# Kernel optimization log

Hardware: AMD Instinct MI355X
Metric: run time of the kernel (lower is better)

## Reference

```python
import jax, jax.numpy as jnp
import numpy as np

B, V, SX, SY, TIN = 4, 3, 256, 256, 10
WIDTH, M1, M2, STEP, VOUT, NL = 32, 16, 16, 10, 3, 6


def setup_inputs() -> dict:
    key = jax.random.key(0)
    ks = jax.random.split(key, 20)
    n = lambda k, s, sc=1.0: sc * jax.random.normal(k, s, dtype=jnp.float32)
    u = lambda k, s: jax.random.uniform(k, s, dtype=jnp.float32)
    sc = 1.0 / WIDTH
    cshape = (NL, WIDTH, WIDTH, V, M1, M2)
    return {
        'x': n(ks[0], (B, V, SX, SY, TIN)),
        'fc0_w': n(ks[1], (TIN + 2, WIDTH), 0.1), 'fc0_b': jnp.zeros((WIDTH,), jnp.float32),
        'w1r': sc * u(ks[2], cshape), 'w1i': sc * u(ks[3], cshape),
        'w2r': sc * u(ks[4], cshape), 'w2i': sc * u(ks[5], cshape),
        'm1w': n(ks[6], (NL, WIDTH, WIDTH), 0.05), 'm1b': jnp.zeros((NL, WIDTH), jnp.float32),
        'm2w': n(ks[7], (NL, WIDTH, WIDTH), 0.05), 'm2b': jnp.zeros((NL, WIDTH), jnp.float32),
        'ww': n(ks[8], (NL, WIDTH, WIDTH), 0.05), 'wb': jnp.zeros((NL, WIDTH), jnp.float32),
        'bw': n(ks[9], (NL, WIDTH, 2), 0.1), 'bb': jnp.zeros((NL, WIDTH), jnp.float32),
        'fc1v_w': n(ks[10], (V, VOUT), 0.3), 'fc1v_b': jnp.zeros((VOUT,), jnp.float32),
        'fc1t_w': n(ks[11], (WIDTH, 256), 0.05), 'fc1t_b': jnp.zeros((256,), jnp.float32),
        'fc2t_w': n(ks[12], (256, STEP), 0.05), 'fc2t_b': jnp.zeros((STEP,), jnp.float32),
    }


def _gelu(t):
    return jax.nn.gelu(t, approximate=False)  # torch F.gelu default = exact erf


def _conv1x1(x, w, b):
    # 1x1x1 Conv3d: channel mix only. x: (b,c,v,x,y), w: (out,in)
    return jnp.einsum('bcvxy,oc->bovxy', x, w) + b[None, :, None, None, None]


def _spectral(x, w1, w2):
    # x: (b,c,v,X,Y); rfft2 over (X,Y); mode-truncated complex mix, zero-pad, irfft2
    sx, sy = x.shape[-2], x.shape[-1]
    xf = jnp.fft.rfft2(x)  # (b,c,v,X,Y//2+1) complex64
    o1 = jnp.einsum('bivxy,iovxy->bovxy', xf[..., :M1, :M2], w1)
    o2 = jnp.einsum('bivxy,iovxy->bovxy', xf[..., -M1:, :M2], w2)
    out = jnp.zeros((x.shape[0], w1.shape[1]) + xf.shape[2:], jnp.complex64)
    out = out.at[..., :M1, :M2].set(o1).at[..., -M1:, :M2].set(o2)
    return jnp.fft.irfft2(out, s=(sx, sy))


def reference(x, fc0_w, fc0_b, w1r, w1i, w2r, w2i, m1w, m1b, m2w, m2b, ww, wb, bw, bb,
              fc1v_w, fc1v_b, fc1t_w, fc1t_b, fc2t_w, fc2t_b):
    b, v, sx, sy, _ = x.shape
    gx = jnp.broadcast_to(jnp.linspace(0.0, 1.0, sx, dtype=jnp.float32)[:, None], (sx, sy))
    gy = jnp.broadcast_to(jnp.linspace(0.0, 1.0, sy, dtype=jnp.float32)[None, :], (sx, sy))
    grid = jnp.broadcast_to(jnp.stack([gx, gy], -1)[None, None], (b, v, sx, sy, 2))
    h = jnp.concatenate([x, grid], -1) @ fc0_w + fc0_b  # (b,v,X,Y,C)
    h = h.transpose(0, 4, 1, 2, 3)  # (b,C,v,X,Y)
    g = grid.transpose(0, 4, 1, 2, 3)  # (b,2,v,X,Y)

    def layer(i, t):
        x1 = _spectral(t, w1r[i] + 1j * w1i[i], w2r[i] + 1j * w2i[i])
        x1 = _conv1x1(_gelu(_conv1x1(x1, m1w[i], m1b[i])), m2w[i], m2b[i])
        x2 = _conv1x1(t, ww[i], wb[i])
        x3 = _conv1x1(g, bw[i], bb[i])
        return _gelu(x1 + x2 + x3)

    h0 = layer(0, h)
    h = layer(1, h0)
    h = layer(2, h) + h0
    h1 = layer(3, h)
    h = layer(4, h1)
    h = layer(5, h) + h1

    h = h.transpose(0, 1, 3, 4, 2)  # (b,C,X,Y,v)
    h = _gelu(h @ fc1v_w + fc1v_b)
    h = h.transpose(0, 4, 2, 3, 1)  # (b,vout,X,Y,C)
    h = _gelu(h @ fc1t_w + fc1t_b)
    return h @ fc2t_w + fc2t_b  # (b,vout,X,Y,step)
```

## Files before the change

### kernel.cpp

```cpp
#include <hip/hip_runtime.h>
#include <math.h>


#define OFF_A   0
#define OFF_B   25165824
#define OFF_T   50331648
#define OFF_XF  53477376
#define OFF_T1  54263808
#define OFF_T2T 54272000
#define OFF_TCS 54288384
#define OFF_TB  54304768
#define OFF_WT  54312960
#define OFF_FW  54321152
#define FWSZ    4718592
#define WS_NEED_WT   ((size_t)OFF_FW * 4)
#define WS_NEED_FOLD ((size_t)(OFF_FW + 4*FWSZ) * 4)

__device__ __forceinline__ float geluf(float x) {
    float a = fabsf(x) * 0.70710678118654752f;
    float t = __builtin_amdgcn_rcpf(fmaf(0.3275911f, a, 1.0f));
    float p = t * fmaf(t, fmaf(t, fmaf(t, fmaf(t, 1.061405429f, -1.453152027f),
                                       1.421413741f), -0.284496736f), 0.254829592f);
    float e = __expf(-a * a);
    float erfa = fmaf(-p, e, 1.0f);
    float er = copysignf(erfa, x);
    return 0.5f * x * (1.0f + er);
}

__global__ void k_init_tables(float* __restrict__ ws, const float* __restrict__ w1t, int do_wt) {
    const float W0 = 6.2831853071795864769f / 256.0f;
    int stride = gridDim.x * blockDim.x;
    int tid = blockIdx.x * blockDim.x + threadIdx.x;
    for (int i = tid; i < 4096; i += stride) {
        int m = i >> 5, q = i & 31, g = q >> 2, j = q & 3;
        int k0 = 4 * (g & 3) + (g >> 2);
        int k = k0 + 2 * (j >> 1);
        float th = W0 * (float)((k * m) & 255);
        ws[OFF_T1 + i] = (j & 1) ? -sinf(th) : cosf(th);
    }
    for (int idx = tid; idx < 8192; idx += stride) {
        int n = idx >> 5, kx = idx & 31;
        int KX = (kx < 16) ? kx : (kx + 224);
        float th = W0 * (float)((KX * n) & 255);
        ws[OFF_T2T + 2*idx]     = cosf(th);
        ws[OFF_T2T + 2*idx + 1] = sinf(th);
    }
    for (int idx = tid; idx < 8192; idx += stride) {
        int kx = idx >> 8, n = idx & 255;
        int KX = (kx < 16) ? kx : (kx + 224);
        float th = W0 * (float)((KX * n) & 255);
        ws[OFF_TCS + 2*idx]     = cosf(th);
        ws[OFF_TCS + 2*idx + 1] = sinf(th);
    }
    for (int idx = tid; idx < 8192; idx += stride) {
        int j = idx >> 8, m = idx & 255, k = j >> 1;
        float th = W0 * (float)((k * m) & 255);
        float beta = (k == 0) ? (1.0f/65536.0f) : (2.0f/65536.0f);
        float val;
        if (j & 1) val = (k == 0) ? 0.0f : -beta * sinf(th);
        else       val = beta * cosf(th);
        ws[OFF_TB + idx] = val;
    }
    if (do_wt) {
        for (int idx = tid; idx < 8192; idx += stride)
            ws[OFF_WT + idx] = w1t[(idx & 31) * 256 + (idx >> 5)];
    }
}

__global__ __launch_bounds__(256) void k_foldw(const float* __restrict__ w1r,
                                               const float* __restrict__ w1i,
                                               const float* __restrict__ w2r,
                                               const float* __restrict__ w2i,
                                               const float* __restrict__ m1w,
                                               float2* __restrict__ fp1,
                                               float2* __restrict__ fp2) {
    int blk = blockIdx.x;
    int p = threadIdx.x;
    int op = blk & 31; int li = blk >> 5;
    int l = li >> 5;
    const float* mrow = m1w + l*1024 + op*32;
#pragma unroll
    for (int v = 0; v < 3; ++v) {
        float a1r = 0.f, a1i = 0.f, a2r = 0.f, a2i = 0.f;
#pragma unroll 4
        for (int o = 0; o < 32; ++o) {
            float mw = mrow[o];
            size_t idx = ((size_t)(li*32 + o)*3 + v)*256 + p;
            a1r = fmaf(mw, w1r[idx], a1r); a1i = fmaf(mw, w1i[idx], a1i);
            a2r = fmaf(mw, w2r[idx], a2r); a2i = fmaf(mw, w2i[idx], a2i);
        }
        size_t oidx = ((size_t)(li*32 + op)*3 + v)*256 + p;
        float2 u1; u1.x = a1r; u1.y = a1i;
        float2 u2; u2.x = a2r; u2.y = a2i;
        fp1[oidx] = u1; fp2[oidx] = u2;
    }
}

__device__ __forceinline__ void fold_lds(float* lds, int tid) {
#pragma unroll
    for (int it = 0; it < 16; ++it) {
        int pi = it * 256 + tid;
        int r = pi >> 7, mm = pi & 127;
        float* row = lds + r * 257;
        float a = row[mm], c = row[mm + 128];
        row[mm] = a + c; row[mm + 128] = a - c;
    }
}

__device__ __forceinline__ void dft_row_phase(const float* lds, const float* __restrict__ tabF,
                                              float* __restrict__ T, int b, int v, int n, int tid) {
    int r = tid >> 3, g = tid & 7;
    int p = g >> 2, idx = g & 3;
    const float* dp = lds + r * 257 + p * 128;
    const float* tp = tabF + g * 4;
    float a0 = 0.f, a1 = 0.f, a2 = 0.f, a3 = 0.f;
#pragma unroll 4
    for (int m = 0; m < 128; ++m) {
        float d = dp[m];
        float4 t = *(const float4*)(tp + m * 32);
        a0 += d * t.x; a1 += d * t.y; a2 += d * t.z; a3 += d * t.w;
    }
    size_t trow = ((size_t)((b * 32 + r) * 3 + v) * 256 + n) * 32;
    float2 w0; w0.x = a0; w0.y = a1;
    float2 w1; w1.x = a2; w1.y = a3;
    *(float2*)(T + trow + 8 * idx + 2 * p) = w0;
    *(float2*)(T + trow + 8 * idx + 2 * p + 4) = w1;
}

__global__ __launch_bounds__(256) void k_fc0(const float* __restrict__ x,
                                             const float* __restrict__ w,
                                             const float* __restrict__ bias,
                                             float* __restrict__ outA,
                                             float* __restrict__ T,
                                             const float* __restrict__ tabF) {
    __shared__ float lds[32 * 257];
    int blk = blockIdx.x;
    int m = threadIdx.x;
    int n = blk & 255;
    int bv = blk >> 8;
    int v = bv % 3, b = bv / 3;
    const float* xp = x + ((size_t)blk * 256 + m) * 10;
    float xin[10];
#pragma unroll
    for (int t = 0; t < 10; t++) xin[t] = xp[t];
    float gx = (float)n * (1.0f/255.0f), gy = (float)m * (1.0f/255.0f);
    float* op = outA + ((size_t)(b*96) + v) * 65536 + n * 256 + m;
#pragma unroll
    for (int c = 0; c < 32; c++) {
        float a = bias[c] + gx * w[10*32 + c] + gy * w[11*32 + c];
#pragma unroll
        for (int t = 0; t < 10; t++) a += xin[t] * w[t*32 + c];
        op[(size_t)c * 196608] = a;
        lds[c * 257 + m] = a;
    }
    __syncthreads();
    fold_lds(lds, m);
    __syncthreads();
    dft_row_phase(lds, tabF, T, b, v, n, m);
}

__global__ __launch_bounds__(256) void k_dft_x(const float* __restrict__ T,
                                               float* __restrict__ XFp,
                                               const float* __restrict__ tab2) {
    __shared__ float lds[4096];
    int idx = blockIdx.x;
    int half = idx & 1; int blk = idx >> 1;
    int i = blk & 31; int bv = blk >> 5;
    int b = bv / 3, v = bv - 3*b;
    int tid = threadIdx.x;
    const float4* slab = (const float4*)(T + (size_t)((b*32 + i)*3 + v) * 8192 + half * 4096);
#pragma unroll
    for (int j = 0; j < 4; ++j)
        ((float4*)lds)[j * 256 + tid] = slab[j * 256 + tid];
    __syncthreads();
    int ky = tid & 15, kxh = tid >> 4;
    const float* t2b = tab2 + half * 128 * 64;
    float r0=0.f, i0=0.f, r1=0.f, i1=0.f;
#pragma unroll 2
    for (int nn = 0; nn < 128; nn++) {
        float2 t = *(const float2*)(lds + nn * 32 + 2 * ky);
        float2 cs0 = *(const float2*)(t2b + nn*64 + kxh*2);
        float2 cs1 = *(const float2*)(t2b + nn*64 + (kxh+16)*2);
        r0 += t.x*cs0.x + t.y*cs0.y;  i0 += t.y*cs0.x - t.x*cs0.y;
        r1 += t.x*cs1.x + t.y*cs1.y;  i1 += t.y*cs1.x - t.x*cs1.y;
    }
    float2* xfp = (float2*)(XFp + (size_t)(half * 384 + blk) * 1024);
    float2 v0; v0.x = r0; v0.y = i0;
    float2 v1; v1.x = r1; v1.y = i1;
    xfp[kxh*16 + ky] = v0;
    xfp[(kxh+16)*16 + ky] = v1;
}

template<int FOLDW>
__global__ __launch_bounds__(256) void k_mixidft(const float* __restrict__ XFp,
                                                 float* __restrict__ T2B,
                                                 const float* __restrict__ w1r,
                                                 const float* __restrict__ w1i,
                                                 const float* __restrict__ w2r,
                                                 const float* __restrict__ w2i,
                                                 const float2* __restrict__ fp1,
                                                 const float2* __restrict__ fp2,
                                                 const float2* __restrict__ tcs, int l) {
    __shared__ float Olds[2048];
    int idx = blockIdx.x;
    int half = idx & 1; int blk = idx >> 1;
    int o = blk & 31; int bv = blk >> 5;
    int b = bv / 3, v = bv - 3*b;
    int tid = threadIdx.x;
    {
        int ky = tid & 15, kxh = tid >> 4;
        float R0=0.f, I0=0.f, R1=0.f, I1=0.f;
#pragma unroll
        for (int i = 0; i < 32; i++) {
            const float2* xa = (const float2*)(XFp + (size_t)(bv*32 + i) * 1024);
            const float2* xb = (const float2*)(XFp + (size_t)(384 + bv*32 + i) * 1024);
            float2 p0 = xa[kxh*16 + ky], q0 = xb[kxh*16 + ky];
            float2 p1 = xa[(kxh+16)*16 + ky], q1 = xb[(kxh+16)*16 + ky];
            float2 xf0; xf0.x = p0.x + q0.x; xf0.y = p0.y + q0.y;
            float2 xf1; xf1.x = p1.x + q1.x; xf1.y = p1.y + q1.y;
            size_t wbase = ((size_t)((l*32 + i)*32 + o)*3 + v) * 256;
            float a1r, a1i, a2r, a2i;
            if (FOLDW) {
                float2 u1 = fp1[wbase + tid]; float2 u2 = fp2[wbase + tid];
                a1r = u1.x; a1i = u1.y; a2r = u2.x; a2i = u2.y;
            } else {
                a1r = w1r[wbase + tid]; a1i = w1i[wbase + tid];
                a2r = w2r[wbase + tid]; a2i = w2i[wbase + tid];
            }
            R0 += xf0.x*a1r - xf0.y*a1i;  I0 += xf0.x*a1i + xf0.y*a1r;
            R1 += xf1.x*a2r - xf1.y*a2i;  I1 += xf1.x*a2i + xf1.y*a2r;
        }
        float2 v0; v0.x = R0; v0.y = I0;
        float2 v1; v1.x = R1; v1.y = I1;
        ((float2*)Olds)[kxh*16 + ky] = v0;
        ((float2*)Olds)[(kxh+16)*16 + ky] = v1;
    }
    __syncthreads();
    {
        int ky2 = tid & 31, n8 = tid >> 5;
        int ky = ky2 >> 1, ri = ky2 & 1;
        float* base = T2B + (size_t)(b*3 + v) * 262144 + o*32;
#pragma unroll 2
        for (int ii = 0; ii < 16; ++ii) {
            int n = half * 128 + ii*8 + n8;
            float acc = 0.f;
#pragma unroll
            for (int kx = 0; kx < 32; ++kx) {
                float2 ov = ((const float2*)Olds)[kx*16 + ky];
                float2 cs = tcs[kx*256 + n];
                float ca = ri ? cs.y : cs.x;
                float cb = ri ? cs.x : -cs.y;
                acc += ov.x*ca + ov.y*cb;
            }
            base[(size_t)n*1024 + ky2] = acc;
        }
    }
}

template<int HAS_SKIP, int DO_DFT, int FOLDED>
__global__ __launch_bounds__(256) void k_conv(
    const float* IN, float* OUT, const float* SK,
    const float* __restrict__ T2B, const float* __restrict__ tabB,
    const float* __restrict__ m1w, const float* __restrict__ m1b,
    const float* __restrict__ m2w, const float* __restrict__ m2b,
    const float* __restrict__ ww,  const float* __restrict__ wb,
    const float* __restrict__ bw,  const float* __restrict__ bb,
    float* __restrict__ Tout, const float* __restrict__ tabF, int l)
{
    __shared__ float lds[DO_DFT ? 32 * 257 : 1];
    int blk = blockIdx.x;
    int m = threadIdx.x;
    int n = blk & 255; int bv = blk >> 8;
    int b = bv / 3, v = bv - 3*b;

    float tb[32];
#pragma unroll
    for (int j = 0; j < 32; j++) tb[j] = tabB[j*256 + m];
    const float* t2row = T2B + (size_t)(bv) * 262144 + (size_t)n * 1024;
    const float* m1bl = m1b + l*32;
    float acc[32];
#pragma unroll
    for (int o = 0; o < 32; o++) {
        const float4* q = (const float4*)(t2row + o*32);
        float a = 0.f;
#pragma unroll
        for (int jj = 0; jj < 8; jj++) {
            float4 qv = q[jj];
            a = fmaf(qv.x, tb[jj*4+0], a);
            a = fmaf(qv.y, tb[jj*4+1], a);
            a = fmaf(qv.z, tb[jj*4+2], a);
            a = fmaf(qv.w, tb[jj*4+3], a);
        }
        acc[o] = a;
    }

    const float* inp = IN + (size_t)(b*96 + v) * 65536 + n * 256 + m;
    float hv[32];
#pragma unroll
    for (int c = 0; c < 32; c++) hv[c] = inp[(size_t)c * 196608];

    float g1[32];
    if (FOLDED) {
#pragma unroll
        for (int o = 0; o < 32; o++) g1[o] = geluf(acc[o] + m1bl[o]);
    } else {
        const float* m1wl = m1w + l*1024;
#pragma unroll
        for (int o = 0; o < 32; o++) {
            const float4* mq = (const float4*)(m1wl + o*32);
            float a = m1bl[o];
#pragma unroll
            for (int c4 = 0; c4 < 8; c4++) {
                float4 wv = mq[c4];
                a = fmaf(wv.x, acc[c4*4+0], a);
                a = fmaf(wv.y, acc[c4*4+1], a);
                a = fmaf(wv.z, acc[c4*4+2], a);
                a = fmaf(wv.w, acc[c4*4+3], a);
            }
            g1[o] = geluf(a);
        }
    }

    const float* m2wl = m2w + l*1024; const float* m2bl = m2b + l*32;
    const float* wwl  = ww  + l*1024; const float* wbl  = wb  + l*32;
    const float* bwl  = bw  + l*64;   const float* bbl  = bb  + l*32;
    float gx = (float)n * (1.0f/255.0f), gy = (float)m * (1.0f/255.0f);
    float* outp = OUT + (size_t)(b*96 + v) * 65536 + n * 256 + m;
    const float* skp = SK + (size_t)(b*96 + v) * 65536 + n * 256 + m;

#pragma unroll
    for (int o = 0; o < 32; o++) {
        const float4* mq = (const float4*)(m2wl + o*32);
        const float4* wq = (const float4*)(wwl + o*32);
        float a = m2bl[o] + wbl[o] + bbl[o] + bwl[o*2]*gx + bwl[o*2+1]*gy;
#pragma unroll
        for (int c4 = 0; c4 < 8; c4++) {
            float4 wv = mq[c4];
            a = fmaf(wv.x, g1[c4*4+0], a);
            a = fmaf(wv.y, g1[c4*4+1], a);
            a = fmaf(wv.z, g1[c4*4+2], a);
            a = fmaf(wv.w, g1[c4*4+3], a);
        }
#pragma unroll
        for (int c4 = 0; c4 < 8; c4++) {
            float4 wv = wq[c4];
            a = fmaf(wv.x, hv[c4*4+0], a);
            a = fmaf(wv.y, hv[c4*4+1], a);
            a = fmaf(wv.z, hv[c4*4+2], a);
            a = fmaf(wv.w, hv[c4*4+3], a);
        }
        float val = geluf(a);
        if (HAS_SKIP) val += skp[(size_t)o * 196608];
        outp[(size_t)o * 196608] = val;
        if (DO_DFT) lds[o * 257 + m] = val;
    }
    if (DO_DFT) {
        __syncthreads();
        fold_lds(lds, m);
        __syncthreads();
        dft_row_phase(lds, tabF, Tout, b, v, n, m);
    }
}

template<int TR>
__global__ __launch_bounds__(256) void k_final(
    const float* __restrict__ IN, float* __restrict__ OUT,
    const float* __restrict__ w1v, const float* __restrict__ b1v,
    const float* __restrict__ w1t, const float* __restrict__ b1t,
    const float* __restrict__ w2t, const float* __restrict__ b2t)
{
    int blk = blockIdx.x;
    int m = threadIdx.x;
    int vo = blk % 3; int rest = blk / 3;
    int n = rest & 255, b = rest >> 8;
    const float* inp = IN + (size_t)(b*96) * 65536 + n * 256 + m;

    float wv0 = w1v[vo], wv1 = w1v[3 + vo], wv2 = w1v[6 + vo], bv0 = b1v[vo];
    float Av[32];
#pragma unroll
    for (int c = 0; c < 32; c++) {
        float f0 = inp[(size_t)(c*3 + 0) * 65536];
        float f1 = inp[(size_t)(c*3 + 1) * 65536];
        float f2 = inp[(size_t)(c*3 + 2) * 65536];
        Av[c] = geluf(f0*wv0 + f1*wv1 + f2*wv2 + bv0);
    }

    float acc[10];
#pragma unroll
    for (int s = 0; s < 10; s++) acc[s] = 0.f;

#pragma unroll 4
    for (int u = 0; u < 256; u++) {
        float t = b1t[u];
        if (TR) {
            const float4* wr = (const float4*)(w1t + u*32);
#pragma unroll
            for (int c4 = 0; c4 < 8; c4++) {
                float4 wv = wr[c4];
                t = fmaf(Av[c4*4+0], wv.x, t);
                t = fmaf(Av[c4*4+1], wv.y, t);
                t = fmaf(Av[c4*4+2], wv.z, t);
                t = fmaf(Av[c4*4+3], wv.w, t);
            }
        } else {
#pragma unroll
            for (int c = 0; c < 32; c++) t = fmaf(Av[c], w1t[c*256 + u], t);
        }
        t = geluf(t);
#pragma unroll
        for (int s = 0; s < 10; s++) acc[s] = fmaf(t, w2t[u*10 + s], acc[s]);
    }

    float* outp = OUT + ((size_t)(b*3 + vo) * 65536 + (size_t)(n * 256 + m)) * 10;
#pragma unroll
    for (int s = 0; s < 10; s++) outp[s] = acc[s] + b2t[s];
}

extern "C" void kernel_launch(void* const* d_in, const int* in_sizes, int n_in,
                              void* d_out, int out_size, void* d_ws, size_t ws_size,
                              hipStream_t stream) {
    const float* x    = (const float*)d_in[0];
    const float* fc0w = (const float*)d_in[1];
    const float* fc0b = (const float*)d_in[2];
    const float* w1r  = (const float*)d_in[3];
    const float* w1i  = (const float*)d_in[4];
    const float* w2r  = (const float*)d_in[5];
    const float* w2i  = (const float*)d_in[6];
    const float* m1w  = (const float*)d_in[7];
    const float* m1b  = (const float*)d_in[8];
    const float* m2w  = (const float*)d_in[9];
    const float* m2b  = (const float*)d_in[10];
    const float* ww   = (const float*)d_in[11];
    const float* wb   = (const float*)d_in[12];
    const float* bw   = (const float*)d_in[13];
    const float* bb   = (const float*)d_in[14];
    const float* w1v  = (const float*)d_in[15];
    const float* b1v  = (const float*)d_in[16];
    const float* w1t  = (const float*)d_in[17];
    const float* b1t  = (const float*)d_in[18];
    const float* w2t  = (const float*)d_in[19];
    const float* b2t  = (const float*)d_in[20];

    float* ws   = (float*)d_ws;
    float* A    = ws + OFF_A;
    float* Bu   = ws + OFF_B;
    float* T    = ws + OFF_T;
    float* XFp  = ws + OFF_XF;
    float* tabF = ws + OFF_T1;
    float* tab2 = ws + OFF_T2T;
    const float2* tcs = (const float2*)(ws + OFF_TCS);
    float* tbB  = ws + OFF_TB;
    float* w1tT = ws + OFF_WT;

    float* T2B = (float*)d_out;

    const bool do_wt = ws_size >= WS_NEED_WT;
    const bool fold  = ws_size >= WS_NEED_FOLD;
    float2* fp1 = (float2*)(ws + OFF_FW);
    float2* fp2 = (float2*)(ws + OFF_FW + 2*FWSZ);

    k_init_tables<<<64, 256, 0, stream>>>(ws, w1t, do_wt ? 1 : 0);
    if (fold)
        k_foldw<<<6144, 256, 0, stream>>>(w1r, w1i, w2r, w2i, m1w, fp1, fp2);
    k_fc0<<<3072, 256, 0, stream>>>(x, fc0w, fc0b, A, T, tabF);

    float* lin [6] = {A, A, Bu, Bu, A, Bu};
    float* lout[6] = {A, Bu, Bu, A, Bu, Bu};
    const float* lskip[6] = {nullptr, nullptr, A, nullptr, nullptr, A};

    for (int l = 0; l < 6; l++) {
        k_dft_x<<<768, 256, 0, stream>>>(T, XFp, tab2);
        if (fold)
            k_mixidft<1><<<768, 256, 0, stream>>>(XFp, T2B, w1r, w1i, w2r, w2i, fp1, fp2, tcs, l);
        else
            k_mixidft<0><<<768, 256, 0, stream>>>(XFp, T2B, w1r, w1i, w2r, w2i, fp1, fp2, tcs, l);
        int skip = lskip[l] != nullptr, dodft = (l < 5);
        if (fold) {
            if (skip && dodft)
                k_conv<1,1,1><<<3072, 256, 0, stream>>>(lin[l], lout[l], lskip[l], T2B, tbB,
                                                        m1w, m1b, m2w, m2b, ww, wb, bw, bb, T, tabF, l);
            else if (!skip && dodft)
                k_conv<0,1,1><<<3072, 256, 0, stream>>>(lin[l], lout[l], nullptr, T2B, tbB,
                                                        m1w, m1b, m2w, m2b, ww, wb, bw, bb, T, tabF, l);
            else if (skip && !dodft)
                k_conv<1,0,1><<<3072, 256, 0, stream>>>(lin[l], lout[l], lskip[l], T2B, tbB,
                                                        m1w, m1b, m2w, m2b, ww, wb, bw, bb, T, tabF, l);
            else
                k_conv<0,0,1><<<3072, 256, 0, stream>>>(lin[l], lout[l], nullptr, T2B, tbB,
                                                        m1w, m1b, m2w, m2b, ww, wb, bw, bb, T, tabF, l);
        } else {
            if (skip && dodft)
                k_conv<1,1,0><<<3072, 256, 0, stream>>>(lin[l], lout[l], lskip[l], T2B, tbB,
                                                        m1w, m1b, m2w, m2b, ww, wb, bw, bb, T, tabF, l);
            else if (!skip && dodft)
                k_conv<0,1,0><<<3072, 256, 0, stream>>>(lin[l], lout[l], nullptr, T2B, tbB,
                                                        m1w, m1b, m2w, m2b, ww, wb, bw, bb, T, tabF, l);
            else if (skip && !dodft)
                k_conv<1,0,0><<<3072, 256, 0, stream>>>(lin[l], lout[l], lskip[l], T2B, tbB,
                                                        m1w, m1b, m2w, m2b, ww, wb, bw, bb, T, tabF, l);
            else
                k_conv<0,0,0><<<3072, 256, 0, stream>>>(lin[l], lout[l], nullptr, T2B, tbB,
                                                        m1w, m1b, m2w, m2b, ww, wb, bw, bb, T, tabF, l);
        }
    }

    if (do_wt)
        k_final<1><<<3072, 256, 0, stream>>>(Bu, (float*)d_out, w1v, b1v, w1tT, b1t, w2t, b2t);
    else
        k_final<0><<<3072, 256, 0, stream>>>(Bu, (float*)d_out, w1v, b1v, w1t, b1t, w2t, b2t);
}
```

Baseline: 2.582 ms.

## Fold m1w into spectral weights per layer and split DFT stages four ways

```diff
diff --git a/kernel.cpp b/kernel.cpp
--- a/kernel.cpp
+++ b/kernel.cpp
@@ -4,17 +4,16 @@
 
 #define OFF_A   0
 #define OFF_B   25165824
-#define OFF_T   50331648
-#define OFF_XF  53477376
-#define OFF_T1  54263808
-#define OFF_T2T 54272000
-#define OFF_TCS 54288384
-#define OFF_TB  54304768
-#define OFF_WT  54312960
-#define OFF_FW  54321152
-#define FWSZ    4718592
-#define WS_NEED_WT   ((size_t)OFF_FW * 4)
-#define WS_NEED_FOLD ((size_t)(OFF_FW + 4*FWSZ) * 4)
+#define OFF_T1  50331648
+#define OFF_T2T 50335744
+#define OFF_TCS 50352128
+#define OFF_TB  50368512
+#define OFF_WT  50376704
+#define OFF_FL  50384896
+
+#define DO_T    0
+#define DO_T2B  3145728
+#define DO_XF   6291456
 
 __device__ __forceinline__ float geluf(float x) {
     float a = fabsf(x) * 0.70710678118654752f;
@@ -27,7 +26,7 @@
     return 0.5f * x * (1.0f + er);
 }
 
-__global__ void k_init_tables(float* __restrict__ ws, const float* __restrict__ w1t, int do_wt) {
+__global__ void k_init_tables(float* __restrict__ ws, const float* __restrict__ w1t) {
     const float W0 = 6.2831853071795864769f / 256.0f;
     int stride = gridDim.x * blockDim.x;
     int tid = blockIdx.x * blockDim.x + threadIdx.x;
@@ -61,35 +60,32 @@
         else       val = beta * cosf(th);
         ws[OFF_TB + idx] = val;
     }
-    if (do_wt) {
-        for (int idx = tid; idx < 8192; idx += stride)
-            ws[OFF_WT + idx] = w1t[(idx & 31) * 256 + (idx >> 5)];
-    }
-}
-
-__global__ __launch_bounds__(256) void k_foldw(const float* __restrict__ w1r,
-                                               const float* __restrict__ w1i,
-                                               const float* __restrict__ w2r,
-                                               const float* __restrict__ w2i,
-                                               const float* __restrict__ m1w,
+    for (int idx = tid; idx < 8192; idx += stride)
+        ws[OFF_WT + idx] = w1t[(idx & 31) * 256 + (idx >> 5)];
+}
+
+__global__ __launch_bounds__(256) void k_foldw(const float* __restrict__ w1r_l,
+                                               const float* __restrict__ w1i_l,
+                                               const float* __restrict__ w2r_l,
+                                               const float* __restrict__ w2i_l,
+                                               const float* __restrict__ m1w_l,
                                                float2* __restrict__ fp1,
                                                float2* __restrict__ fp2) {
     int blk = blockIdx.x;
     int p = threadIdx.x;
-    int op = blk & 31; int li = blk >> 5;
-    int l = li >> 5;
-    const float* mrow = m1w + l*1024 + op*32;
+    int op = blk & 31; int i = blk >> 5;
+    const float* mrow = m1w_l + op*32;
 #pragma unroll
     for (int v = 0; v < 3; ++v) {
         float a1r = 0.f, a1i = 0.f, a2r = 0.f, a2i = 0.f;
 #pragma unroll 4
         for (int o = 0; o < 32; ++o) {
             float mw = mrow[o];
-            size_t idx = ((size_t)(li*32 + o)*3 + v)*256 + p;
-            a1r = fmaf(mw, w1r[idx], a1r); a1i = fmaf(mw, w1i[idx], a1i);
-            a2r = fmaf(mw, w2r[idx], a2r); a2i = fmaf(mw, w2i[idx], a2i);
-        }
-        size_t oidx = ((size_t)(li*32 + op)*3 + v)*256 + p;
+            size_t idx = ((size_t)(i*32 + o)*3 + v)*256 + p;
+            a1r = fmaf(mw, w1r_l[idx], a1r); a1i = fmaf(mw, w1i_l[idx], a1i);
+            a2r = fmaf(mw, w2r_l[idx], a2r); a2i = fmaf(mw, w2i_l[idx], a2i);
+        }
+        size_t oidx = ((size_t)(i*32 + op)*3 + v)*256 + p;
         float2 u1; u1.x = a1r; u1.y = a1i;
         float2 u2; u2.x = a2r; u2.y = a2i;
         fp1[oidx] = u1; fp2[oidx] = u2;
@@ -162,73 +158,65 @@
 __global__ __launch_bounds__(256) void k_dft_x(const float* __restrict__ T,
                                                float* __restrict__ XFp,
                                                const float* __restrict__ tab2) {
-    __shared__ float lds[4096];
+    __shared__ float lds[2048];
     int idx = blockIdx.x;
-    int half = idx & 1; int blk = idx >> 1;
+    int part = idx & 3; int blk = idx >> 2;
     int i = blk & 31; int bv = blk >> 5;
     int b = bv / 3, v = bv - 3*b;
     int tid = threadIdx.x;
-    const float4* slab = (const float4*)(T + (size_t)((b*32 + i)*3 + v) * 8192 + half * 4096);
-#pragma unroll
-    for (int j = 0; j < 4; ++j)
+    const float4* slab = (const float4*)(T + (size_t)((b*32 + i)*3 + v) * 8192 + part * 2048);
+#pragma unroll
+    for (int j = 0; j < 2; ++j)
         ((float4*)lds)[j * 256 + tid] = slab[j * 256 + tid];
     __syncthreads();
     int ky = tid & 15, kxh = tid >> 4;
-    const float* t2b = tab2 + half * 128 * 64;
+    const float* t2b = tab2 + part * 4096;
     float r0=0.f, i0=0.f, r1=0.f, i1=0.f;
 #pragma unroll 2
-    for (int nn = 0; nn < 128; nn++) {
+    for (int nn = 0; nn < 64; nn++) {
         float2 t = *(const float2*)(lds + nn * 32 + 2 * ky);
         float2 cs0 = *(const float2*)(t2b + nn*64 + kxh*2);
         float2 cs1 = *(const float2*)(t2b + nn*64 + (kxh+16)*2);
         r0 += t.x*cs0.x + t.y*cs0.y;  i0 += t.y*cs0.x - t.x*cs0.y;
         r1 += t.x*cs1.x + t.y*cs1.y;  i1 += t.y*cs1.x - t.x*cs1.y;
     }
-    float2* xfp = (float2*)(XFp + (size_t)(half * 384 + blk) * 1024);
+    float2* xfp = (float2*)(XFp + (size_t)part * 393216 + (size_t)blk * 1024);
     float2 v0; v0.x = r0; v0.y = i0;
     float2 v1; v1.x = r1; v1.y = i1;
     xfp[kxh*16 + ky] = v0;
     xfp[(kxh+16)*16 + ky] = v1;
 }
 
-template<int FOLDW>
 __global__ __launch_bounds__(256) void k_mixidft(const float* __restrict__ XFp,
                                                  float* __restrict__ T2B,
-                                                 const float* __restrict__ w1r,
-                                                 const float* __restrict__ w1i,
-                                                 const float* __restrict__ w2r,
-                                                 const float* __restrict__ w2i,
                                                  const float2* __restrict__ fp1,
                                                  const float2* __restrict__ fp2,
-                                                 const float2* __restrict__ tcs, int l) {
+                                                 const float2* __restrict__ tcs) {
     __shared__ float Olds[2048];
     int idx = blockIdx.x;
-    int half = idx & 1; int blk = idx >> 1;
+    int part = idx & 3; int blk = idx >> 2;
     int o = blk & 31; int bv = blk >> 5;
     int b = bv / 3, v = bv - 3*b;
     int tid = threadIdx.x;
     {
         int ky = tid & 15, kxh = tid >> 4;
         float R0=0.f, I0=0.f, R1=0.f, I1=0.f;
-#pragma unroll
+#pragma unroll 4
         for (int i = 0; i < 32; i++) {
-            const float2* xa = (const float2*)(XFp + (size_t)(bv*32 + i) * 1024);
-            const float2* xb = (const float2*)(XFp + (size_t)(384 + bv*32 + i) * 1024);
-            float2 p0 = xa[kxh*16 + ky], q0 = xb[kxh*16 + ky];
-            float2 p1 = xa[(kxh+16)*16 + ky], q1 = xb[(kxh+16)*16 + ky];
-            float2 xf0; xf0.x = p0.x + q0.x; xf0.y = p0.y + q0.y;
-            float2 xf1; xf1.x = p1.x + q1.x; xf1.y = p1.y + q1.y;
-            size_t wbase = ((size_t)((l*32 + i)*32 + o)*3 + v) * 256;
-            float a1r, a1i, a2r, a2i;
-            if (FOLDW) {
-                float2 u1 = fp1[wbase + tid]; float2 u2 = fp2[wbase + tid];
-                a1r = u1.x; a1i = u1.y; a2r = u2.x; a2i = u2.y;
-            } else {
-                a1r = w1r[wbase + tid]; a1i = w1i[wbase + tid];
-                a2r = w2r[wbase + tid]; a2i = w2i[wbase + tid];
+            size_t xbase = (size_t)(bv*32 + i) * 1024;
+            float x0r=0.f, x0i=0.f, x1r=0.f, x1i=0.f;
+#pragma unroll
+            for (int p = 0; p < 4; p++) {
+                const float2* xp = (const float2*)(XFp + (size_t)p * 393216 + xbase);
+                float2 a = xp[kxh*16 + ky];
+                float2 c = xp[(kxh+16)*16 + ky];
+                x0r += a.x; x0i += a.y; x1r += c.x; x1i += c.y;
             }
-            R0 += xf0.x*a1r - xf0.y*a1i;  I0 += xf0.x*a1i + xf0.y*a1r;
-            R1 += xf1.x*a2r - xf1.y*a2i;  I1 += xf1.x*a2i + xf1.y*a2r;
+            size_t wbase = ((size_t)(i*32 + o)*3 + v) * 256;
+            float2 u1 = fp1[wbase + tid];
+            float2 u2 = fp2[wbase + tid];
+            R0 += x0r*u1.x - x0i*u1.y;  I0 += x0r*u1.y + x0i*u1.x;
+            R1 += x1r*u2.x - x1i*u2.y;  I1 += x1r*u2.y + x1i*u2.x;
         }
         float2 v0; v0.x = R0; v0.y = I0;
         float2 v1; v1.x = R1; v1.y = I1;
@@ -239,10 +227,10 @@
     {
         int ky2 = tid & 31, n8 = tid >> 5;
         int ky = ky2 >> 1, ri = ky2 & 1;
-        float* base = T2B + (size_t)(b*3 + v) * 262144 + o*32;
+        float* base = T2B + (size_t)bv * 262144 + o*32;
 #pragma unroll 2
-        for (int ii = 0; ii < 16; ++ii) {
-            int n = half * 128 + ii*8 + n8;
+        for (int ii = 0; ii < 8; ++ii) {
+            int n = part*64 + ii*8 + n8;
             float acc = 0.f;
 #pragma unroll
             for (int kx = 0; kx < 32; ++kx) {
@@ -257,11 +245,11 @@
     }
 }
 
-template<int HAS_SKIP, int DO_DFT, int FOLDED>
+template<int HAS_SKIP, int DO_DFT>
 __global__ __launch_bounds__(256) void k_conv(
     const float* IN, float* OUT, const float* SK,
     const float* __restrict__ T2B, const float* __restrict__ tabB,
-    const float* __restrict__ m1w, const float* __restrict__ m1b,
+    const float* __restrict__ m1b,
     const float* __restrict__ m2w, const float* __restrict__ m2b,
     const float* __restrict__ ww,  const float* __restrict__ wb,
     const float* __restrict__ bw,  const float* __restrict__ bb,
@@ -276,13 +264,18 @@
     float tb[32];
 #pragma unroll
     for (int j = 0; j < 32; j++) tb[j] = tabB[j*256 + m];
-    const float* t2row = T2B + (size_t)(bv) * 262144 + (size_t)n * 1024;
+    const float* inp = IN + (size_t)(b*96 + v) * 65536 + n * 256 + m;
+    float hv[32];
+#pragma unroll
+    for (int c = 0; c < 32; c++) hv[c] = inp[(size_t)c * 196608];
+
+    const float* t2row = T2B + (size_t)bv * 262144 + (size_t)n * 1024;
     const float* m1bl = m1b + l*32;
-    float acc[32];
+    float g1[32];
 #pragma unroll
     for (int o = 0; o < 32; o++) {
         const float4* q = (const float4*)(t2row + o*32);
-        float a = 0.f;
+        float a = m1bl[o];
 #pragma unroll
         for (int jj = 0; jj < 8; jj++) {
             float4 qv = q[jj];
@@ -291,34 +284,7 @@
             a = fmaf(qv.z, tb[jj*4+2], a);
             a = fmaf(qv.w, tb[jj*4+3], a);
         }
-        acc[o] = a;
-    }
-
-    const float* inp = IN + (size_t)(b*96 + v) * 65536 + n * 256 + m;
-    float hv[32];
-#pragma unroll
-    for (int c = 0; c < 32; c++) hv[c] = inp[(size_t)c * 196608];
-
-    float g1[32];
-    if (FOLDED) {
-#pragma unroll
-        for (int o = 0; o < 32; o++) g1[o] = geluf(acc[o] + m1bl[o]);
-    } else {
-        const float* m1wl = m1w + l*1024;
-#pragma unroll
-        for (int o = 0; o < 32; o++) {
-            const float4* mq = (const float4*)(m1wl + o*32);
-            float a = m1bl[o];
-#pragma unroll
-            for (int c4 = 0; c4 < 8; c4++) {
-                float4 wv = mq[c4];
-                a = fmaf(wv.x, acc[c4*4+0], a);
-                a = fmaf(wv.y, acc[c4*4+1], a);
-                a = fmaf(wv.z, acc[c4*4+2], a);
-                a = fmaf(wv.w, acc[c4*4+3], a);
-            }
-            g1[o] = geluf(a);
-        }
+        g1[o] = geluf(a);
     }
 
     const float* m2wl = m2w + l*1024; const float* m2bl = m2b + l*32;
@@ -362,11 +328,10 @@
     }
 }
 
-template<int TR>
 __global__ __launch_bounds__(256) void k_final(
     const float* __restrict__ IN, float* __restrict__ OUT,
     const float* __restrict__ w1v, const float* __restrict__ b1v,
-    const float* __restrict__ w1t, const float* __restrict__ b1t,
+    const float* __restrict__ w1tT, const float* __restrict__ b1t,
     const float* __restrict__ w2t, const float* __restrict__ b2t)
 {
     int blk = blockIdx.x;
@@ -392,19 +357,14 @@
 #pragma unroll 4
     for (int u = 0; u < 256; u++) {
         float t = b1t[u];
-        if (TR) {
-            const float4* wr = (const float4*)(w1t + u*32);
-#pragma unroll
-            for (int c4 = 0; c4 < 8; c4++) {
-                float4 wv = wr[c4];
-                t = fmaf(Av[c4*4+0], wv.x, t);
-                t = fmaf(Av[c4*4+1], wv.y, t);
-                t = fmaf(Av[c4*4+2], wv.z, t);
-                t = fmaf(Av[c4*4+3], wv.w, t);
-            }
-        } else {
-#pragma unroll
-            for (int c = 0; c < 32; c++) t = fmaf(Av[c], w1t[c*256 + u], t);
+        const float4* wr = (const float4*)(w1tT + u*32);
+#pragma unroll
+        for (int c4 = 0; c4 < 8; c4++) {
+            float4 wv = wr[c4];
+            t = fmaf(Av[c4*4+0], wv.x, t);
+            t = fmaf(Av[c4*4+1], wv.y, t);
+            t = fmaf(Av[c4*4+2], wv.z, t);
+            t = fmaf(Av[c4*4+3], wv.w, t);
         }
         t = geluf(t);
 #pragma unroll
@@ -444,24 +404,20 @@
     float* ws   = (float*)d_ws;
     float* A    = ws + OFF_A;
     float* Bu   = ws + OFF_B;
-    float* T    = ws + OFF_T;
-    float* XFp  = ws + OFF_XF;
     float* tabF = ws + OFF_T1;
     float* tab2 = ws + OFF_T2T;
     const float2* tcs = (const float2*)(ws + OFF_TCS);
     float* tbB  = ws + OFF_TB;
     float* w1tT = ws + OFF_WT;
-
-    float* T2B = (float*)d_out;
-
-    const bool do_wt = ws_size >= WS_NEED_WT;
-    const bool fold  = ws_size >= WS_NEED_FOLD;
-    float2* fp1 = (float2*)(ws + OFF_FW);
-    float2* fp2 = (float2*)(ws + OFF_FW + 2*FWSZ);
-
-    k_init_tables<<<64, 256, 0, stream>>>(ws, w1t, do_wt ? 1 : 0);
-    if (fold)
-        k_foldw<<<6144, 256, 0, stream>>>(w1r, w1i, w2r, w2i, m1w, fp1, fp2);
+    float2* fp1 = (float2*)(ws + OFF_FL);
+    float2* fp2 = (float2*)(ws + OFF_FL + 1572864);
+
+    float* dout = (float*)d_out;
+    float* T    = dout + DO_T;
+    float* T2B  = dout + DO_T2B;
+    float* XFp  = dout + DO_XF;
+
+    k_init_tables<<<64, 256, 0, stream>>>(ws, w1t);
     k_fc0<<<3072, 256, 0, stream>>>(x, fc0w, fc0b, A, T, tabF);
 
     float* lin [6] = {A, A, Bu, Bu, A, Bu};
@@ -469,43 +425,25 @@
     const float* lskip[6] = {nullptr, nullptr, A, nullptr, nullptr, A};
 
     for (int l = 0; l < 6; l++) {
-        k_dft_x<<<768, 256, 0, stream>>>(T, XFp, tab2);
-        if (fold)
-            k_mixidft<1><<<768, 256, 0, stream>>>(XFp, T2B, w1r, w1i, w2r, w2i, fp1, fp2, tcs, l);
+        k_foldw<<<1024, 256, 0, stream>>>(w1r + (size_t)l*786432, w1i + (size_t)l*786432,
+                                          w2r + (size_t)l*786432, w2i + (size_t)l*786432,
+                                          m1w + l*1024, fp1, fp2);
+        k_dft_x<<<1536, 256, 0, stream>>>(T, XFp, tab2);
+        k_mixidft<<<1536, 256, 0, stream>>>(XFp, T2B, fp1, fp2, tcs);
+        int skip = lskip[l] != nullptr, dodft = (l < 5);
+        if (skip && dodft)
+            k_conv<1,1><<<3072, 256, 0, stream>>>(lin[l], lout[l], lskip[l], T2B, tbB,
+                                                  m1b, m2w, m2b, ww, wb, bw, bb, T, tabF, l);
+        else if (!skip && dodft)
+            k_conv<0,1><<<3072, 256, 0, stream>>>(lin[l], lout[l], nullptr, T2B, tbB,
+                                                  m1b, m2w, m2b, ww, wb, bw, bb, T, tabF, l);
+        else if (skip && !dodft)
+            k_conv<1,0><<<3072, 256, 0, stream>>>(lin[l], lout[l], lskip[l], T2B, tbB,
+                                                  m1b, m2w, m2b, ww, wb, bw, bb, T, tabF, l);
         else
-            k_mixidft<0><<<768, 256, 0, stream>>>(XFp, T2B, w1r, w1i, w2r, w2i, fp1, fp2, tcs, l);
-        int skip = lskip[l] != nullptr, dodft = (l < 5);
-        if (fold) {
-            if (skip && dodft)
-                k_conv<1,1,1><<<3072, 256, 0, stream>>>(lin[l], lout[l], lskip[l], T2B, tbB,
-                                                        m1w, m1b, m2w, m2b, ww, wb, bw, bb, T, tabF, l);
-            else if (!skip && dodft)
-                k_conv<0,1,1><<<3072, 256, 0, stream>>>(lin[l], lout[l], nullptr, T2B, tbB,
-                                                        m1w, m1b, m2w, m2b, ww, wb, bw, bb, T, tabF, l);
-            else if (skip && !dodft)
-                k_conv<1,0,1><<<3072, 256, 0, stream>>>(lin[l], lout[l], lskip[l], T2B, tbB,
-                                                        m1w, m1b, m2w, m2b, ww, wb, bw, bb, T, tabF, l);
-            else
-                k_conv<0,0,1><<<3072, 256, 0, stream>>>(lin[l], lout[l], nullptr, T2B, tbB,
-                                                        m1w, m1b, m2w, m2b, ww, wb, bw, bb, T, tabF, l);
-        } else {
-            if (skip && dodft)
-                k_conv<1,1,0><<<3072, 256, 0, stream>>>(lin[l], lout[l], lskip[l], T2B, tbB,
-                                                        m1w, m1b, m2w, m2b, ww, wb, bw, bb, T, tabF, l);
-            else if (!skip && dodft)
-                k_conv<0,1,0><<<3072, 256, 0, stream>>>(lin[l], lout[l], nullptr, T2B, tbB,
-                                                        m1w, m1b, m2w, m2b, ww, wb, bw, bb, T, tabF, l);
-            else if (skip && !dodft)
-                k_conv<1,0,0><<<3072, 256, 0, stream>>>(lin[l], lout[l], lskip[l], T2B, tbB,
-                                                        m1w, m1b, m2w, m2b, ww, wb, bw, bb, T, tabF, l);
-            else
-                k_conv<0,0,0><<<3072, 256, 0, stream>>>(lin[l], lout[l], nullptr, T2B, tbB,
-                                                        m1w, m1b, m2w, m2b, ww, wb, bw, bb, T, tabF, l);
-        }
-    }
-
-    if (do_wt)
-        k_final<1><<<3072, 256, 0, stream>>>(Bu, (float*)d_out, w1v, b1v, w1tT, b1t, w2t, b2t);
-    else
-        k_final<0><<<3072, 256, 0, stream>>>(Bu, (float*)d_out, w1v, b1v, w1t, b1t, w2t, b2t);
-}
+            k_conv<0,0><<<3072, 256, 0, stream>>>(lin[l], lout[l], nullptr, T2B, tbB,
+                                                  m1b, m2w, m2b, ww, wb, bw, bb, T, tabF, l);
+    }
+
+    k_final<<<3072, 256, 0, stream>>>(Bu, dout, w1v, b1v, w1tT, b1t, w2t, b2t);
+}
```

Result: slower. 2.717 ms (+5.2%).
